# Kernel optimization log

Measured on AMD Instinct MI355X. Metric: run time of the kernel, lower is better.

Reference implementation:

```python
import jax, jax.numpy as jnp
import numpy as np
import math

B, T, M, C, H = 4, 1024, 256, 512, 8
HD = C // H
NEG = -1e30


def setup_inputs() -> dict:
    key = jax.random.key(0)
    ks = jax.random.split(key, 16)
    s = 1.0 / math.sqrt(C)
    inp = {
        'x': jax.random.normal(ks[0], (B, T, C), jnp.float32),
        'y': jax.random.normal(ks[1], (B, M, C), jnp.float32),
        'attn_x_mask': jnp.tril(jnp.ones((T, T), bool))[None, None],  # causal (1,1,T,T)
        'Wqkv_x': jax.random.normal(ks[2], (C, 3 * C), jnp.float32) * s,
        'bqkv_x': jnp.zeros((3 * C,), jnp.float32),
        'Wqkv_y': jax.random.normal(ks[3], (C, 3 * C), jnp.float32) * s,
        'bqkv_y': jnp.zeros((3 * C,), jnp.float32),
        'w4x': jax.random.normal(ks[4], (H, HD), jnp.float32) * math.sqrt(1.0 / C / 3),
        'w4y': jax.random.normal(ks[5], (H, HD), jnp.float32) * math.sqrt(1.0 / C / 3),
        'w4xy': jax.random.normal(ks[6], (H, HD), jnp.float32) * math.sqrt(1.0 / C / 3),
        'Wgs': jax.random.normal(ks[7], (C, C), jnp.float32) * s,
        'bgs': jnp.zeros((C,), jnp.float32),
        'Wgc': jax.random.normal(ks[8], (C, C), jnp.float32) * s,
        'bgc': jnp.zeros((C,), jnp.float32),
        'Wp': jax.random.normal(ks[9], (C, C), jnp.float32) * s,
        'bp': jnp.zeros((C,), jnp.float32),
    }
    return inp


def _heads(t):
    b, n, c = t.shape
    return t.reshape(b, n, H, HD).transpose(0, 2, 1, 3)  # (B,H,N,HD)


def reference(x, y, attn_x_mask, Wqkv_x, bqkv_x, Wqkv_y, bqkv_y,
              w4x, w4y, w4xy, Wgs, bgs, Wgc, bgc, Wp, bp):
    q_x, k_x, v_x = [_heads(t) for t in jnp.split(x @ Wqkv_x + bqkv_x, 3, axis=-1)]
    q_y, k_y, v_y = [_heads(t) for t in jnp.split(y @ Wqkv_y + bqkv_y, 3, axis=-1)]
    scale = 1.0 / math.sqrt(HD)

    # additive bias attention: catt1 (per query-x), catt2 (per key-y), catt3 (bilinear)
    catt1 = jnp.einsum('bhtd,hd->bht', q_x, w4x)[..., :, None]          # (B,H,T,1)
    catt2 = jnp.einsum('bhmd,hd->bhm', q_y, w4y)[:, :, None, :]          # (B,H,1,M)
    catt3 = jnp.einsum('bhtd,bhmd->bhtm', q_x * w4xy[None, :, None, :], k_y) * scale
    catt = catt1 + catt2 + catt3                                         # (B,H,T,M)

    catt_x2y = jax.nn.softmax(catt, axis=-1)
    catt_y2x = jax.nn.softmax(catt, axis=-2)

    cval_x2y = jnp.einsum('bhtm,bhmd->bhtd', catt_x2y, v_y)
    cval_x2y = cval_x2y.transpose(0, 2, 1, 3).reshape(B, T, C)

    # product-of-attentions: (T,M) @ (M,T) -> (T,T)
    chain = jnp.einsum('bhtm,bhsm->bhts', catt_x2y, catt_y2x) * (1.0 / math.sqrt(M))
    chain = jnp.where(attn_x_mask, chain, NEG)
    chain = jax.nn.softmax(chain, axis=-1)
    cval_y2x = jnp.einsum('bhts,bhsd->bhtd', chain, v_x)
    cval_y2x = cval_y2x.transpose(0, 2, 1, 3).reshape(B, T, C)

    cval = cval_x2y + cval_y2x + x

    # masked self-attention
    satt = jnp.einsum('bhtd,bhsd->bhts', q_x, k_x) * scale
    satt = jnp.where(attn_x_mask, satt, NEG)
    satt = jax.nn.softmax(satt, axis=-1)
    sval = jnp.einsum('bhts,bhsd->bhtd', satt, v_x).transpose(0, 2, 1, 3).reshape(B, T, C)

    sgate = jax.nn.sigmoid(sval @ Wgs + bgs)
    cgate = jax.nn.sigmoid(cval @ Wgc + bgc)
    out = (sgate * cval + cgate * sval) @ Wp + bp
    return out
```

## Files before the change

### kernel.cpp

```cpp
#include <hip/hip_runtime.h>
#include <hip/hip_bf16.h>

typedef __hip_bfloat16 bf16;
using f4 = __attribute__((ext_vector_type(4))) float;
using s8 = __attribute__((ext_vector_type(8))) short;
using s4 = __attribute__((ext_vector_type(4))) short;

__device__ __forceinline__ void storeOut(float* p, float v) { *p = v; }
__device__ __forceinline__ void storeOut(bf16* p, float v) { *p = __float2bfloat16(v); }
__device__ __forceinline__ short bfs(float x) { return __builtin_bit_cast(short, __float2bfloat16(x)); }

constexpr int B_ = 4, T_ = 1024, M_ = 256, C_ = 512, H_ = 8, HD_ = 64, C3_ = 1536;

#define MFMA16(a, b, c) __builtin_amdgcn_mfma_f32_16x16x32_bf16((a), (b), (c), 0, 0, 0)

__global__ __launch_bounds__(256) void prep_kernel(
    const float* __restrict__ Wqkv_x, const float* __restrict__ Wqkv_y,
    const float* __restrict__ Wgs, const float* __restrict__ Wgc, const float* __restrict__ Wp,
    const float* __restrict__ x, const float* __restrict__ y,
    bf16* __restrict__ WT_x, bf16* __restrict__ WT_y, bf16* __restrict__ WT_gs,
    bf16* __restrict__ WT_gc, bf16* __restrict__ WT_p,
    bf16* __restrict__ x_bf, bf16* __restrict__ y_bf)
{
    __shared__ float Ls[64][65];
    const int tid = threadIdx.x;
    const int bid = blockIdx.x;
    if (bid < 576) {
        const float* W; bf16* WT; int N, t;
        if (bid < 192)      { W = Wqkv_x; WT = WT_x;  N = C3_; t = bid; }
        else if (bid < 384) { W = Wqkv_y; WT = WT_y;  N = C3_; t = bid - 192; }
        else if (bid < 448) { W = Wgs;    WT = WT_gs; N = C_;  t = bid - 384; }
        else if (bid < 512) { W = Wgc;    WT = WT_gc; N = C_;  t = bid - 448; }
        else                { W = Wp;     WT = WT_p;  N = C_;  t = bid - 512; }
        const int K = C_;
        const int tw = N >> 6;
        const int n0 = (t % tw) * 64, k0 = (t / tw) * 64;
        for (int i = tid; i < 1024; i += 256) {
            int kr = i >> 4, ng = i & 15;
            float4 v = *(const float4*)&W[(size_t)(k0 + kr) * N + n0 + ng * 4];
            Ls[ng * 4 + 0][kr] = v.x; Ls[ng * 4 + 1][kr] = v.y;
            Ls[ng * 4 + 2][kr] = v.z; Ls[ng * 4 + 3][kr] = v.w;
        }
        __syncthreads();
        for (int i = tid; i < 512; i += 256) {
            int n = i >> 3, kg = i & 7;
            s8 r;
            #pragma unroll
            for (int j = 0; j < 8; ++j) r[j] = bfs(Ls[n][kg * 8 + j]);
            *(s8*)&WT[(size_t)(n0 + n) * K + k0 + kg * 8] = r;
        }
    } else if (bid < 1600) {
        int i = (bid - 576) * 2048 + tid * 8;
        s8 r;
        #pragma unroll
        for (int j = 0; j < 8; ++j) r[j] = bfs(x[i + j]);
        *(s8*)&x_bf[i] = r;
    } else {
        int i = (bid - 1600) * 2048 + tid * 8;
        s8 r;
        #pragma unroll
        for (int j = 0; j < 8; ++j) r[j] = bfs(y[i + j]);
        *(s8*)&y_bf[i] = r;
    }
}

__global__ __launch_bounds__(256) void qwcatt_kernel(
    const bf16* __restrict__ qkv_x, const bf16* __restrict__ qkv_y,
    const float* __restrict__ w4x, const float* __restrict__ w4y,
    const float* __restrict__ w4xy,
    float* __restrict__ catt1b, float* __restrict__ catt2b, bf16* __restrict__ qw)
{
    const int bid = blockIdx.x;
    const int tid = threadIdx.x;
    if (bid < 160) {
        int i = bid * 256 + tid;
        const bf16* row; const float* w; float* out; int oi;
        if (i < 32768) {
            int bh = i >> 10, t = i & 1023, b = bh >> 3, h = bh & 7;
            row = qkv_x + (size_t)(b * T_ + t) * C3_ + h * HD_;
            w = w4x + h * HD_; out = catt1b; oi = i;
        } else {
            int j = i - 32768;
            int bh = j >> 8, m = j & 255, b = bh >> 3, h = bh & 7;
            row = qkv_y + (size_t)(b * M_ + m) * C3_ + h * HD_;
            w = w4y + h * HD_; out = catt2b; oi = j;
        }
        float s = 0.f;
        #pragma unroll
        for (int d = 0; d < HD_; ++d) s = fmaf(__bfloat162float(row[d]), w[d], s);
        out[oi] = s;
    } else {
        int o = ((bid - 160) * 256 + tid) * 8;
        int row = o >> 9, c = o & 511;
        const bf16* src = qkv_x + (size_t)row * C3_ + c;
        s8 r;
        #pragma unroll
        for (int j = 0; j < 8; ++j) r[j] = bfs(__bfloat162float(src[j]) * w4xy[c + j]);
        *(s8*)&qw[o] = r;
    }
}

template <typename OT>
__global__ __launch_bounds__(256) void gemm_staged_kernel(
    const bf16* __restrict__ A, const bf16* __restrict__ WT, const float* __restrict__ bias,
    OT* __restrict__ Cmat, int N, int K)
{
    __shared__ short Asb[128][72];
    __shared__ short Bsb[64][72];
    const int tid = threadIdx.x;
    const int wave = tid >> 6, lane = tid & 63;
    const int quad = lane >> 4, l16 = lane & 15;
    const int n0 = blockIdx.y * 64, m0 = blockIdx.x * 128;
    f4 acc[2][4];
    #pragma unroll
    for (int mt = 0; mt < 2; ++mt)
        #pragma unroll
        for (int nt = 0; nt < 4; ++nt) acc[mt][nt] = (f4)0.f;

    for (int k0 = 0; k0 < K; k0 += 64) {
        #pragma unroll
        for (int tl = 0; tl < 4; ++tl) {
            int g = tid + tl * 256, row = g >> 3, grp = g & 7;
            *(s8*)&Asb[row][grp * 8] = *(const s8*)&A[(size_t)(m0 + row) * K + k0 + grp * 8];
        }
        #pragma unroll
        for (int tl = 0; tl < 2; ++tl) {
            int g = tid + tl * 256, n = g >> 3, grp = g & 7;
            *(s8*)&Bsb[n][grp * 8] = *(const s8*)&WT[(size_t)(n0 + n) * K + k0 + grp * 8];
        }
        __syncthreads();
        #pragma unroll
        for (int ks = 0; ks < 2; ++ks) {
            s8 a0 = *(const s8*)&Asb[wave * 32 + l16][ks * 32 + quad * 8];
            s8 a1 = *(const s8*)&Asb[wave * 32 + 16 + l16][ks * 32 + quad * 8];
            #pragma unroll
            for (int nt = 0; nt < 4; ++nt) {
                s8 bv = *(const s8*)&Bsb[nt * 16 + l16][ks * 32 + quad * 8];
                acc[0][nt] = MFMA16(a0, bv, acc[0][nt]);
                acc[1][nt] = MFMA16(a1, bv, acc[1][nt]);
            }
        }
        __syncthreads();
    }
    #pragma unroll
    for (int mt = 0; mt < 2; ++mt)
        #pragma unroll
        for (int nt = 0; nt < 4; ++nt) {
            int col = n0 + nt * 16 + l16;
            float bb = bias[col];
            #pragma unroll
            for (int reg = 0; reg < 4; ++reg) {
                int row = m0 + wave * 32 + mt * 16 + quad * 4 + reg;
                storeOut(&Cmat[(size_t)row * N + col], acc[mt][nt][reg] + bb);
            }
        }
}

__global__ __launch_bounds__(256) void catt3r_kernel(
    const bf16* __restrict__ qw, const bf16* __restrict__ qkv_y,
    const float* __restrict__ catt1, const float* __restrict__ catt2,
    bf16* __restrict__ x2y, float* __restrict__ rowsum_, float* __restrict__ psum)
{
    __shared__ float redc[4][256];
    const int tid = threadIdx.x;
    const int wave = tid >> 6, lane = tid & 63;
    const int quad = lane >> 4, l16 = lane & 15;
    const int bh = blockIdx.x, b = bh >> 3, h = bh & 7;
    const int t0 = blockIdx.y * 64;
    f4 sc[4][4];
    #pragma unroll
    for (int mt = 0; mt < 4; ++mt)
        #pragma unroll
        for (int nt = 0; nt < 4; ++nt) sc[mt][nt] = (f4)0.f;

    const bf16* ap = qw + (size_t)(b * T_ + t0 + wave * 16 + l16) * C_ + h * HD_ + quad * 8;
    s8 a0 = *(const s8*)ap;
    s8 a1 = *(const s8*)(ap + 32);
    const bf16* bp = qkv_y + (size_t)(b * M_ + l16) * C3_ + C_ + h * HD_ + quad * 8;
    #pragma unroll
    for (int mt = 0; mt < 4; ++mt)
        #pragma unroll
        for (int nt = 0; nt < 4; ++nt) {
            const bf16* bq = bp + (size_t)(mt * 64 + nt * 16) * C3_;
            sc[mt][nt] = MFMA16(a0, *(const s8*)bq, sc[mt][nt]);
            sc[mt][nt] = MFMA16(a1, *(const s8*)(bq + 32), sc[mt][nt]);
        }

    float c1[4];
    #pragma unroll
    for (int reg = 0; reg < 4; ++reg)
        c1[reg] = catt1[bh * T_ + t0 + wave * 16 + quad * 4 + reg];
    #pragma unroll
    for (int mt = 0; mt < 4; ++mt)
        #pragma unroll
        for (int nt = 0; nt < 4; ++nt) {
            float c2 = catt2[bh * M_ + mt * 64 + nt * 16 + l16];
            #pragma unroll
            for (int reg = 0; reg < 4; ++reg)
                sc[mt][nt][reg] = __expf(sc[mt][nt][reg] * 0.125f + c1[reg] + c2);
        }

    #pragma unroll
    for (int reg = 0; reg < 4; ++reg) {
        float rs = 0.f;
        #pragma unroll
        for (int mt = 0; mt < 4; ++mt)
            #pragma unroll
            for (int nt = 0; nt < 4; ++nt) rs += sc[mt][nt][reg];
        rs += __shfl_xor(rs, 1); rs += __shfl_xor(rs, 2);
        rs += __shfl_xor(rs, 4); rs += __shfl_xor(rs, 8);
        const int t = t0 + wave * 16 + quad * 4 + reg;
        if (l16 == 0) rowsum_[bh * T_ + t] = rs;
        const float ri = 1.f / rs;
        #pragma unroll
        for (int mt = 0; mt < 4; ++mt)
            #pragma unroll
            for (int nt = 0; nt < 4; ++nt)
                x2y[((size_t)bh * T_ + t) * M_ + mt * 64 + nt * 16 + l16] =
                    __float2bfloat16(sc[mt][nt][reg] * ri);
    }

    #pragma unroll
    for (int mt = 0; mt < 4; ++mt)
        #pragma unroll
        for (int nt = 0; nt < 4; ++nt) {
            float es = sc[mt][nt][0] + sc[mt][nt][1] + sc[mt][nt][2] + sc[mt][nt][3];
            es += __shfl_xor(es, 16);
            es += __shfl_xor(es, 32);
            if (quad == 0) redc[wave][mt * 64 + nt * 16 + l16] = es;
        }
    __syncthreads();
    psum[((size_t)bh * 16 + blockIdx.y) * M_ + tid] =
        redc[0][tid] + redc[1][tid] + redc[2][tid] + redc[3][tid];
}

__global__ __launch_bounds__(256) void colfin_vtrans_kernel(
    const float* __restrict__ psum, float* __restrict__ colinv,
    const bf16* __restrict__ qkv_x, const bf16* __restrict__ qkv_y,
    bf16* __restrict__ vTx, bf16* __restrict__ vTy)
{
    __shared__ short Ls[64][68];
    const int tid = threadIdx.x;
    int bid = blockIdx.x;
    if (bid < 32) {
        const int bh = bid, m = tid;
        float s = 0.f;
        #pragma unroll
        for (int ch = 0; ch < 16; ++ch) s += psum[(bh * 16 + ch) * M_ + m];
        colinv[bh * M_ + m] = 1.f / s;
        return;
    }
    bid -= 32;
    const bf16* qkv; bf16* vT; int Nrows, bh, t0;
    if (bid < 512) { qkv = qkv_x; vT = vTx; Nrows = T_; bh = bid >> 4; t0 = (bid & 15) * 64; }
    else { bid -= 512; qkv = qkv_y; vT = vTy; Nrows = M_; bh = bid >> 2; t0 = (bid & 3) * 64; }
    const int b = bh >> 3, h = bh & 7;
    for (int i = tid; i < 4096; i += 256) {
        int tl = i >> 6, d = i & 63;
        Ls[d][tl] = __builtin_bit_cast(short,
            qkv[(size_t)(b * Nrows + t0 + tl) * C3_ + 2 * C_ + h * HD_ + d]);
    }
    __syncthreads();
    for (int i = tid; i < 4096; i += 256) {
        int d = i >> 6, tl = i & 63;
        vT[((size_t)bh * 64 + d) * Nrows + t0 + tl] = __builtin_bit_cast(bf16, Ls[d][tl]);
    }
}

__global__ __launch_bounds__(256) void y2xw_kernel(
    const bf16* __restrict__ x2y, const float* __restrict__ rowsum_,
    const float* __restrict__ colinv, bf16* __restrict__ y2x)
{
    const int i = (blockIdx.x * 256 + threadIdx.x) * 8;
    const int row = i >> 8, m = i & 255, bh = row >> 10;
    const float rs = rowsum_[row];
    s8 v = *(const s8*)&x2y[i];
    const float4 c0 = *(const float4*)&colinv[bh * M_ + m];
    const float4 c4 = *(const float4*)&colinv[bh * M_ + m + 4];
    float ci[8] = {c0.x, c0.y, c0.z, c0.w, c4.x, c4.y, c4.z, c4.w};
    s8 r;
    #pragma unroll
    for (int j = 0; j < 8; ++j)
        r[j] = bfs(__bfloat162float(__builtin_bit_cast(bf16, v[j])) * rs * ci[j]);
    *(s8*)&y2x[i] = r;
}

__global__ __launch_bounds__(512) void flash8_kernel(
    const bf16* __restrict__ x2y, const bf16* __restrict__ y2x,
    const bf16* __restrict__ vTx, const bf16* __restrict__ vTy,
    const bf16* __restrict__ qkv_x, const float* __restrict__ x,
    bf16* __restrict__ cval_bf, bf16* __restrict__ sval_bf)
{
    __shared__ short Kc[64][264];
    __shared__ short Ksf[64][72];
    __shared__ short Vb[64][72];
    __shared__ short Ps[8][16][68];
    const int tid = threadIdx.x;
    const int wave = tid >> 6, lane = tid & 63;
    const int quad = lane >> 4, l16 = lane & 15;
    const int bh = blockIdx.x, b = bh >> 3, h = bh & 7;
    const int p = blockIdx.y;
    const int jt = (wave < 4) ? p : (15 - p);
    const int rb = jt * 64 + (wave & 3) * 16;
    const int nst = 16 - p;

    s8 qc[8], qs[2];
    {
        const bf16* qp = x2y + (size_t)(bh * T_ + rb + l16) * M_ + quad * 8;
        #pragma unroll
        for (int f = 0; f < 8; ++f) qc[f] = *(const s8*)(qp + f * 32);
        const bf16* qsp = qkv_x + (size_t)(b * T_ + rb + l16) * C3_ + h * HD_ + quad * 8;
        qs[0] = *(const s8*)qsp;
        qs[1] = *(const s8*)(qsp + 32);
    }

    f4 ocv[4];
    #pragma unroll
    for (int dt = 0; dt < 4; ++dt) ocv[dt] = (f4)0.f;
    {
        const bf16* vb = vTy + (size_t)(bh * 64 + l16) * M_ + quad * 8;
        #pragma unroll
        for (int f = 0; f < 8; ++f)
            #pragma unroll
            for (int dt = 0; dt < 4; ++dt) {
                s8 bv = *(const s8*)(vb + (size_t)dt * 16 * M_ + f * 32);
                ocv[dt] = MFMA16(qc[f], bv, ocv[dt]);
            }
    }

    f4 oc[4], os_[4];
    float lc[4] = {0.f, 0.f, 0.f, 0.f}, ls_[4] = {0.f, 0.f, 0.f, 0.f};
    #pragma unroll
    for (int dt = 0; dt < 4; ++dt) { oc[dt] = (f4)0.f; os_[dt] = (f4)0.f; }

    #pragma unroll
    for (int tl = 0; tl < 4; ++tl) {
        int g = tid + tl * 512, row = g >> 5, grp = g & 31;
        *(s8*)&Kc[row][grp * 8] = *(const s8*)&y2x[(size_t)(bh * T_ + row) * M_ + grp * 8];
    }
    {
        int row = tid >> 3, grp = tid & 7;
        *(s8*)&Ksf[row][grp * 8] =
            *(const s8*)&qkv_x[(size_t)(b * T_ + row) * C3_ + C_ + h * HD_ + grp * 8];
        *(s8*)&Vb[row][grp * 8] = *(const s8*)&vTx[(size_t)(bh * 64 + row) * T_ + grp * 8];
    }
    __syncthreads();

    for (int st = 0; st < nst; ++st) {
        const int s0 = st * 64;
        const bool pf = (st + 1) < nst;
        s8 kcp[4], ksp, vp;
        if (pf) {
            const int sn = s0 + 64;
            #pragma unroll
            for (int tl = 0; tl < 4; ++tl) {
                int g = tid + tl * 512, row = g >> 5, grp = g & 31;
                kcp[tl] = *(const s8*)&y2x[(size_t)(bh * T_ + sn + row) * M_ + grp * 8];
            }
            int row = tid >> 3, grp = tid & 7;
            ksp = *(const s8*)&qkv_x[(size_t)(b * T_ + sn + row) * C3_ + C_ + h * HD_ + grp * 8];
            vp = *(const s8*)&vTx[(size_t)(bh * 64 + row) * T_ + sn + grp * 8];
        }
        if (st <= jt) {
            f4 sc[4];
            #pragma unroll
            for (int nt = 0; nt < 4; ++nt) sc[nt] = (f4)0.f;
            #pragma unroll
            for (int f = 0; f < 8; ++f)
                #pragma unroll
                for (int nt = 0; nt < 4; ++nt) {
                    s8 bv = *(const s8*)&Kc[nt * 16 + l16][f * 32 + quad * 8];
                    sc[nt] = MFMA16(qc[f], bv, sc[nt]);
                }
            f4 ss[4];
            #pragma unroll
            for (int nt = 0; nt < 4; ++nt) ss[nt] = (f4)0.f;
            #pragma unroll
            for (int f = 0; f < 2; ++f)
                #pragma unroll
                for (int nt = 0; nt < 4; ++nt) {
                    s8 bv = *(const s8*)&Ksf[nt * 16 + l16][f * 32 + quad * 8];
                    ss[nt] = MFMA16(qs[f], bv, ss[nt]);
                }
            #pragma unroll
            for (int reg = 0; reg < 4; ++reg) {
                const int t_g = rb + quad * 4 + reg;
                #pragma unroll
                for (int nt = 0; nt < 4; ++nt) {
                    float pv = (s0 + nt * 16 + l16 <= t_g) ? __expf(sc[nt][reg] * (1.f / 16.f)) : 0.f;
                    lc[reg] += pv;
                    Ps[wave][quad * 4 + reg][nt * 16 + l16] = bfs(pv);
                }
            }
            #pragma unroll
            for (int ks = 0; ks < 2; ++ks) {
                const short* pp = &Ps[wave][l16][ks * 32 + quad * 8];
                s4 alo = *(const s4*)pp;
                s4 ahi = *(const s4*)(pp + 4);
                s8 a;
                a[0] = alo[0]; a[1] = alo[1]; a[2] = alo[2]; a[3] = alo[3];
                a[4] = ahi[0]; a[5] = ahi[1]; a[6] = ahi[2]; a[7] = ahi[3];
                #pragma unroll
                for (int dt = 0; dt < 4; ++dt) {
                    s8 bv = *(const s8*)&Vb[dt * 16 + l16][ks * 32 + quad * 8];
                    oc[dt] = MFMA16(a, bv, oc[dt]);
                }
            }
            #pragma unroll
            for (int reg = 0; reg < 4; ++reg) {
                const int t_g = rb + quad * 4 + reg;
                #pragma unroll
                for (int nt = 0; nt < 4; ++nt) {
                    float pv = (s0 + nt * 16 + l16 <= t_g) ? __expf(ss[nt][reg] * 0.125f) : 0.f;
                    ls_[reg] += pv;
                    Ps[wave][quad * 4 + reg][nt * 16 + l16] = bfs(pv);
                }
            }
            #pragma unroll
            for (int ks = 0; ks < 2; ++ks) {
                const short* pp = &Ps[wave][l16][ks * 32 + quad * 8];
                s4 alo = *(const s4*)pp;
                s4 ahi = *(const s4*)(pp + 4);
                s8 a;
                a[0] = alo[0]; a[1] = alo[1]; a[2] = alo[2]; a[3] = alo[3];
                a[4] = ahi[0]; a[5] = ahi[1]; a[6] = ahi[2]; a[7] = ahi[3];
                #pragma unroll
                for (int dt = 0; dt < 4; ++dt) {
                    s8 bv = *(const s8*)&Vb[dt * 16 + l16][ks * 32 + quad * 8];
                    os_[dt] = MFMA16(a, bv, os_[dt]);
                }
            }
        }
        __syncthreads();
        if (pf) {
            #pragma unroll
            for (int tl = 0; tl < 4; ++tl) {
                int g = tid + tl * 512, row = g >> 5, grp = g & 31;
                *(s8*)&Kc[row][grp * 8] = kcp[tl];
            }
            int row = tid >> 3, grp = tid & 7;
            *(s8*)&Ksf[row][grp * 8] = ksp;
            *(s8*)&Vb[row][grp * 8] = vp;
        }
        __syncthreads();
    }

    #pragma unroll
    for (int reg = 0; reg < 4; ++reg) {
        float l1 = lc[reg], l2 = ls_[reg];
        l1 += __shfl_xor(l1, 1); l1 += __shfl_xor(l1, 2);
        l1 += __shfl_xor(l1, 4); l1 += __shfl_xor(l1, 8);
        l2 += __shfl_xor(l2, 1); l2 += __shfl_xor(l2, 2);
        l2 += __shfl_xor(l2, 4); l2 += __shfl_xor(l2, 8);
        const float i1 = 1.f / l1, i2 = 1.f / l2;
        const int t = rb + quad * 4 + reg;
        #pragma unroll
        for (int dt = 0; dt < 4; ++dt) {
            size_t idx = (size_t)(b * T_ + t) * C_ + h * HD_ + dt * 16 + l16;
            float cv = ocv[dt][reg] + oc[dt][reg] * i1 + x[idx];
            cval_bf[idx] = __float2bfloat16(cv);
            float sv = os_[dt][reg] * i2;
            sval_bf[idx] = __float2bfloat16(sv);
        }
    }
}

__global__ __launch_bounds__(256) void gatefuse_kernel(
    const bf16* __restrict__ svalb, const bf16* __restrict__ cvalb,
    const bf16* __restrict__ WTgs, const bf16* __restrict__ WTgc,
    const float* __restrict__ bgs, const float* __restrict__ bgc,
    bf16* __restrict__ gated)
{
    __shared__ short Sb[128][72], Cb[128][72], W1b[64][72], W2b[64][72];
    const int tid = threadIdx.x;
    const int wave = tid >> 6, lane = tid & 63;
    const int quad = lane >> 4, l16 = lane & 15;
    const int n0 = blockIdx.y * 64, m0 = blockIdx.x * 128;
    f4 aS[2][4], aC[2][4];
    #pragma unroll
    for (int mt = 0; mt < 2; ++mt)
        #pragma unroll
        for (int nt = 0; nt < 4; ++nt) { aS[mt][nt] = (f4)0.f; aC[mt][nt] = (f4)0.f; }

    for (int k0 = 0; k0 < C_; k0 += 64) {
        #pragma unroll
        for (int tl = 0; tl < 4; ++tl) {
            int g = tid + tl * 256, row = g >> 3, grp = g & 7;
            *(s8*)&Sb[row][grp * 8] = *(const s8*)&svalb[(size_t)(m0 + row) * C_ + k0 + grp * 8];
            *(s8*)&Cb[row][grp * 8] = *(const s8*)&cvalb[(size_t)(m0 + row) * C_ + k0 + grp * 8];
        }
        #pragma unroll
        for (int tl = 0; tl < 2; ++tl) {
            int g = tid + tl * 256, n = g >> 3, grp = g & 7;
            *(s8*)&W1b[n][grp * 8] = *(const s8*)&WTgs[(size_t)(n0 + n) * C_ + k0 + grp * 8];
            *(s8*)&W2b[n][grp * 8] = *(const s8*)&WTgc[(size_t)(n0 + n) * C_ + k0 + grp * 8];
        }
        __syncthreads();
        #pragma unroll
        for (int ks = 0; ks < 2; ++ks) {
            s8 s0f = *(const s8*)&Sb[wave * 32 + l16][ks * 32 + quad * 8];
            s8 s1f = *(const s8*)&Sb[wave * 32 + 16 + l16][ks * 32 + quad * 8];
            s8 c0f = *(const s8*)&Cb[wave * 32 + l16][ks * 32 + quad * 8];
            s8 c1f = *(const s8*)&Cb[wave * 32 + 16 + l16][ks * 32 + quad * 8];
            #pragma unroll
            for (int nt = 0; nt < 4; ++nt) {
                s8 w1 = *(const s8*)&W1b[nt * 16 + l16][ks * 32 + quad * 8];
                s8 w2 = *(const s8*)&W2b[nt * 16 + l16][ks * 32 + quad * 8];
                aS[0][nt] = MFMA16(s0f, w1, aS[0][nt]);
                aS[1][nt] = MFMA16(s1f, w1, aS[1][nt]);
                aC[0][nt] = MFMA16(c0f, w2, aC[0][nt]);
                aC[1][nt] = MFMA16(c1f, w2, aC[1][nt]);
            }
        }
        __syncthreads();
    }
    #pragma unroll
    for (int mt = 0; mt < 2; ++mt)
        #pragma unroll
        for (int nt = 0; nt < 4; ++nt) {
            int col = n0 + nt * 16 + l16;
            float b1 = bgs[col], b2 = bgc[col];
            #pragma unroll
            for (int reg = 0; reg < 4; ++reg) {
                int row = m0 + wave * 32 + mt * 16 + quad * 4 + reg;
                size_t idx = (size_t)row * C_ + col;
                float gs = 1.f / (1.f + __expf(-(aS[mt][nt][reg] + b1)));
                float gc = 1.f / (1.f + __expf(-(aC[mt][nt][reg] + b2)));
                float cvv = __bfloat162float(cvalb[idx]);
                float svv = __bfloat162float(svalb[idx]);
                gated[idx] = __float2bfloat16(gs * cvv + gc * svv);
            }
        }
}

extern "C" void kernel_launch(void* const* d_in, const int* in_sizes, int n_in,
                              void* d_out, int out_size, void* d_ws, size_t ws_size,
                              hipStream_t stream)
{
    const float* x      = (const float*)d_in[0];
    const float* y      = (const float*)d_in[1];
    const float* Wqkv_x = (const float*)d_in[3];
    const float* bqkv_x = (const float*)d_in[4];
    const float* Wqkv_y = (const float*)d_in[5];
    const float* bqkv_y = (const float*)d_in[6];
    const float* w4x    = (const float*)d_in[7];
    const float* w4y    = (const float*)d_in[8];
    const float* w4xy   = (const float*)d_in[9];
    const float* Wgs    = (const float*)d_in[10];
    const float* bgs    = (const float*)d_in[11];
    const float* Wgc    = (const float*)d_in[12];
    const float* bgc    = (const float*)d_in[13];
    const float* Wp     = (const float*)d_in[14];
    const float* bp     = (const float*)d_in[15];

    float* ws = (float*)d_ws;
    bf16*  qkv_x_bf = (bf16*)(ws + 0);
    bf16*  qkv_y_bf = (bf16*)(ws + 3145728);
    bf16*  gated_bf = (bf16*)(ws + 3932160);
    bf16*  cval_bf  = (bf16*)(ws + 5242880);
    bf16*  x2y_bf   = (bf16*)(ws + 12320768);
    bf16*  x_bf     = x2y_bf;
    bf16*  y_bf     = (bf16*)(ws + 13369344);
    bf16*  y2x_bf   = (bf16*)(ws + 16515072);
    bf16*  vTx_bf   = (bf16*)(ws + 20709376);
    bf16*  vTy_bf   = (bf16*)(ws + 21757952);
    float* psum_    = ws + 22020096;
    bf16*  qw_bf    = (bf16*)(ws + 26214400);
    bf16*  sval_bf  = qw_bf;
    bf16*  WT_x     = (bf16*)(ws + 27262976);
    bf16*  WT_y     = (bf16*)(ws + 27656192);
    bf16*  WT_gs    = (bf16*)(ws + 28049408);
    bf16*  WT_gc    = (bf16*)(ws + 28180480);
    bf16*  WT_p     = (bf16*)(ws + 28311552);
    float* catt1b   = ws + 28442624;
    float* catt2b   = ws + 28475392;
    float* colinv   = ws + 28483584;
    float* rowsum_  = ws + 28491776;

    prep_kernel<<<1856, 256, 0, stream>>>(
        Wqkv_x, Wqkv_y, Wgs, Wgc, Wp, x, y,
        WT_x, WT_y, WT_gs, WT_gc, WT_p, x_bf, y_bf);

    gemm_staged_kernel<bf16><<<dim3(32, 24), 256, 0, stream>>>(x_bf, WT_x, bqkv_x, qkv_x_bf, C3_, C_);
    gemm_staged_kernel<bf16><<<dim3(8, 24), 256, 0, stream>>>(y_bf, WT_y, bqkv_y, qkv_y_bf, C3_, C_);

    qwcatt_kernel<<<1184, 256, 0, stream>>>(
        qkv_x_bf, qkv_y_bf, w4x, w4y, w4xy, catt1b, catt2b, qw_bf);

    catt3r_kernel<<<dim3(32, 16), 256, 0, stream>>>(
        qw_bf, qkv_y_bf, catt1b, catt2b, x2y_bf, rowsum_, psum_);

    colfin_vtrans_kernel<<<672, 256, 0, stream>>>(psum_, colinv, qkv_x_bf, qkv_y_bf, vTx_bf, vTy_bf);

    y2xw_kernel<<<4096, 256, 0, stream>>>(x2y_bf, rowsum_, colinv, y2x_bf);

    flash8_kernel<<<dim3(32, 8), 512, 0, stream>>>(
        x2y_bf, y2x_bf, vTx_bf, vTy_bf, qkv_x_bf, x, cval_bf, sval_bf);

    gatefuse_kernel<<<dim3(32, 8), 256, 0, stream>>>(
        sval_bf, cval_bf, WT_gs, WT_gc, bgs, bgc, gated_bf);

    gemm_staged_kernel<float><<<dim3(32, 8), 256, 0, stream>>>(
        gated_bf, WT_p, bp, (float*)d_out, C_, C_);
}
```

Baseline: 223.0 us.

## Rework flash attention kernel: register P transpose, per-block query tiles, wave priority

Replaces the 512-thread paired-tile flash kernel with a 256-thread kernel where each block owns one 64-row query tile, launched heaviest-first. The MFMA operands are swapped so the score tile comes out transposed, and P is converted to bf16 and rearranged in registers via ds_bpermute instead of a shared-memory round trip. Causal masking is applied only on the diagonal tile, and s_setprio is raised around MFMA bursts. This removes LDS traffic and the per-element mask work but doubles the block count, so K/V tiles are reloaded per block rather than shared across two query tiles.

Measured after the change: 231.8 us. 4.0% more time.

```diff
diff --git a/kernel.cpp b/kernel.cpp
--- a/kernel.cpp
+++ b/kernel.cpp
@@ -5,6 +5,7 @@
 using f4 = __attribute__((ext_vector_type(4))) float;
 using s8 = __attribute__((ext_vector_type(8))) short;
 using s4 = __attribute__((ext_vector_type(4))) short;
+using u4v = __attribute__((ext_vector_type(4))) unsigned;
 
 __device__ __forceinline__ void storeOut(float* p, float v) { *p = v; }
 __device__ __forceinline__ void storeOut(bf16* p, float v) { *p = __float2bfloat16(v); }
@@ -285,7 +286,41 @@
     *(s8*)&y2x[i] = r;
 }
 
-__global__ __launch_bounds__(512) void flash8_kernel(
+__device__ __forceinline__ unsigned cvtpk(float lo, float hi) {
+    unsigned d;
+    asm("v_cvt_pk_bf16_f32 %0, %1, %2" : "=v"(d) : "v"(lo), "v"(hi));
+    return d;
+}
+
+__device__ __forceinline__ void ptrans(const f4* sc, int idx0, int idx1, int gsel,
+                                       s8& aw0, s8& aw1)
+{
+    unsigned pk[4][2];
+    #pragma unroll
+    for (int nt = 0; nt < 4; ++nt) {
+        pk[nt][0] = cvtpk(sc[nt][0], sc[nt][1]);
+        pk[nt][1] = cvtpk(sc[nt][2], sc[nt][3]);
+    }
+    unsigned r[4][2][2];
+    #pragma unroll
+    for (int nt = 0; nt < 4; ++nt)
+        #pragma unroll
+        for (int par = 0; par < 2; ++par) {
+            r[nt][par][0] = (unsigned)__builtin_amdgcn_ds_bpermute(idx0, (int)pk[nt][par]);
+            r[nt][par][1] = (unsigned)__builtin_amdgcn_ds_bpermute(idx1, (int)pk[nt][par]);
+        }
+    u4v w0, w1;
+    #pragma unroll
+    for (int jp = 0; jp < 4; ++jp) {
+        const int par = jp & 1, hh = jp >> 1;
+        w0[jp] = gsel ? r[1][par][hh] : r[0][par][hh];
+        w1[jp] = gsel ? r[3][par][hh] : r[2][par][hh];
+    }
+    aw0 = __builtin_bit_cast(s8, w0);
+    aw1 = __builtin_bit_cast(s8, w1);
+}
+
+__global__ __launch_bounds__(256) void flash9_kernel(
     const bf16* __restrict__ x2y, const bf16* __restrict__ y2x,
     const bf16* __restrict__ vTx, const bf16* __restrict__ vTy,
     const bf16* __restrict__ qkv_x, const float* __restrict__ x,
@@ -294,15 +329,16 @@
     __shared__ short Kc[64][264];
     __shared__ short Ksf[64][72];
     __shared__ short Vb[64][72];
-    __shared__ short Ps[8][16][68];
     const int tid = threadIdx.x;
     const int wave = tid >> 6, lane = tid & 63;
     const int quad = lane >> 4, l16 = lane & 15;
     const int bh = blockIdx.x, b = bh >> 3, h = bh & 7;
-    const int p = blockIdx.y;
-    const int jt = (wave < 4) ? p : (15 - p);
-    const int rb = jt * 64 + (wave & 3) * 16;
-    const int nst = 16 - p;
+    const int jt = (blockIdx.y < 8) ? (15 - (int)blockIdx.y) : ((int)blockIdx.y - 8);
+    const int rb = jt * 64 + wave * 16;
+    const int nst = jt + 1;
+    const int gsel = quad >> 1;
+    const int idx0 = (((quad & 1) * 2) * 16 + l16) * 4;
+    const int idx1 = (((quad & 1) * 2 + 1) * 16 + l16) * 4;
 
     s8 qc[8], qs[2];
     {
@@ -329,17 +365,18 @@
     }
 
     f4 oc[4], os_[4];
-    float lc[4] = {0.f, 0.f, 0.f, 0.f}, ls_[4] = {0.f, 0.f, 0.f, 0.f};
+    float lc = 0.f, ls = 0.f;
     #pragma unroll
     for (int dt = 0; dt < 4; ++dt) { oc[dt] = (f4)0.f; os_[dt] = (f4)0.f; }
 
     #pragma unroll
-    for (int tl = 0; tl < 4; ++tl) {
-        int g = tid + tl * 512, row = g >> 5, grp = g & 31;
+    for (int tl = 0; tl < 8; ++tl) {
+        int g = tid + tl * 256, row = g >> 5, grp = g & 31;
         *(s8*)&Kc[row][grp * 8] = *(const s8*)&y2x[(size_t)(bh * T_ + row) * M_ + grp * 8];
     }
-    {
-        int row = tid >> 3, grp = tid & 7;
+    #pragma unroll
+    for (int tl = 0; tl < 2; ++tl) {
+        int g = tid + tl * 256, row = g >> 3, grp = g & 7;
         *(s8*)&Ksf[row][grp * 8] =
             *(const s8*)&qkv_x[(size_t)(b * T_ + row) * C3_ + C_ + h * HD_ + grp * 8];
         *(s8*)&Vb[row][grp * 8] = *(const s8*)&vTx[(size_t)(bh * 64 + row) * T_ + grp * 8];
@@ -349,110 +386,112 @@
     for (int st = 0; st < nst; ++st) {
         const int s0 = st * 64;
         const bool pf = (st + 1) < nst;
-        s8 kcp[4], ksp, vp;
+        s8 kcp[8], ksp[2], vp[2];
         if (pf) {
             const int sn = s0 + 64;
             #pragma unroll
-            for (int tl = 0; tl < 4; ++tl) {
-                int g = tid + tl * 512, row = g >> 5, grp = g & 31;
+            for (int tl = 0; tl < 8; ++tl) {
+                int g = tid + tl * 256, row = g >> 5, grp = g & 31;
                 kcp[tl] = *(const s8*)&y2x[(size_t)(bh * T_ + sn + row) * M_ + grp * 8];
             }
-            int row = tid >> 3, grp = tid & 7;
-            ksp = *(const s8*)&qkv_x[(size_t)(b * T_ + sn + row) * C3_ + C_ + h * HD_ + grp * 8];
-            vp = *(const s8*)&vTx[(size_t)(bh * 64 + row) * T_ + sn + grp * 8];
-        }
-        if (st <= jt) {
+            #pragma unroll
+            for (int tl = 0; tl < 2; ++tl) {
+                int g = tid + tl * 256, row = g >> 3, grp = g & 7;
+                ksp[tl] = *(const s8*)&qkv_x[(size_t)(b * T_ + sn + row) * C3_ + C_ + h * HD_ + grp * 8];
+                vp[tl] = *(const s8*)&vTx[(size_t)(bh * 64 + row) * T_ + sn + grp * 8];
+            }
+        }
+        {
+            const bool diag = (st == jt);
+            const int t_l = rb + l16;
             f4 sc[4];
             #pragma unroll
             for (int nt = 0; nt < 4; ++nt) sc[nt] = (f4)0.f;
+            __builtin_amdgcn_s_setprio(1);
             #pragma unroll
             for (int f = 0; f < 8; ++f)
                 #pragma unroll
                 for (int nt = 0; nt < 4; ++nt) {
                     s8 bv = *(const s8*)&Kc[nt * 16 + l16][f * 32 + quad * 8];
-                    sc[nt] = MFMA16(qc[f], bv, sc[nt]);
+                    sc[nt] = MFMA16(bv, qc[f], sc[nt]);
                 }
+            __builtin_amdgcn_s_setprio(0);
             f4 ss[4];
             #pragma unroll
             for (int nt = 0; nt < 4; ++nt) ss[nt] = (f4)0.f;
+            __builtin_amdgcn_s_setprio(1);
             #pragma unroll
             for (int f = 0; f < 2; ++f)
                 #pragma unroll
                 for (int nt = 0; nt < 4; ++nt) {
                     s8 bv = *(const s8*)&Ksf[nt * 16 + l16][f * 32 + quad * 8];
-                    ss[nt] = MFMA16(qs[f], bv, ss[nt]);
+                    ss[nt] = MFMA16(bv, qs[f], ss[nt]);
                 }
-            #pragma unroll
-            for (int reg = 0; reg < 4; ++reg) {
-                const int t_g = rb + quad * 4 + reg;
+            __builtin_amdgcn_s_setprio(0);
+            #pragma unroll
+            for (int nt = 0; nt < 4; ++nt)
                 #pragma unroll
-                for (int nt = 0; nt < 4; ++nt) {
-                    float pv = (s0 + nt * 16 + l16 <= t_g) ? __expf(sc[nt][reg] * (1.f / 16.f)) : 0.f;
-                    lc[reg] += pv;
-                    Ps[wave][quad * 4 + reg][nt * 16 + l16] = bfs(pv);
+                for (int reg = 0; reg < 4; ++reg) {
+                    float e = __expf(sc[nt][reg] * 0.0625f);
+                    if (diag) e = (s0 + nt * 16 + quad * 4 + reg <= t_l) ? e : 0.f;
+                    lc += e;
+                    sc[nt][reg] = e;
                 }
-            }
-            #pragma unroll
-            for (int ks = 0; ks < 2; ++ks) {
-                const short* pp = &Ps[wave][l16][ks * 32 + quad * 8];
-                s4 alo = *(const s4*)pp;
-                s4 ahi = *(const s4*)(pp + 4);
-                s8 a;
-                a[0] = alo[0]; a[1] = alo[1]; a[2] = alo[2]; a[3] = alo[3];
-                a[4] = ahi[0]; a[5] = ahi[1]; a[6] = ahi[2]; a[7] = ahi[3];
+            s8 ac0, ac1;
+            ptrans(sc, idx0, idx1, gsel, ac0, ac1);
+            __builtin_amdgcn_s_setprio(1);
+            #pragma unroll
+            for (int dt = 0; dt < 4; ++dt) {
+                s8 bv0 = *(const s8*)&Vb[dt * 16 + l16][quad * 8];
+                oc[dt] = MFMA16(ac0, bv0, oc[dt]);
+                s8 bv1 = *(const s8*)&Vb[dt * 16 + l16][32 + quad * 8];
+                oc[dt] = MFMA16(ac1, bv1, oc[dt]);
+            }
+            __builtin_amdgcn_s_setprio(0);
+            #pragma unroll
+            for (int nt = 0; nt < 4; ++nt)
                 #pragma unroll
-                for (int dt = 0; dt < 4; ++dt) {
-                    s8 bv = *(const s8*)&Vb[dt * 16 + l16][ks * 32 + quad * 8];
-                    oc[dt] = MFMA16(a, bv, oc[dt]);
+                for (int reg = 0; reg < 4; ++reg) {
+                    float e = __expf(ss[nt][reg] * 0.125f);
+                    if (diag) e = (s0 + nt * 16 + quad * 4 + reg <= t_l) ? e : 0.f;
+                    ls += e;
+                    ss[nt][reg] = e;
                 }
-            }
-            #pragma unroll
-            for (int reg = 0; reg < 4; ++reg) {
-                const int t_g = rb + quad * 4 + reg;
-                #pragma unroll
-                for (int nt = 0; nt < 4; ++nt) {
-                    float pv = (s0 + nt * 16 + l16 <= t_g) ? __expf(ss[nt][reg] * 0.125f) : 0.f;
-                    ls_[reg] += pv;
-                    Ps[wave][quad * 4 + reg][nt * 16 + l16] = bfs(pv);
-                }
-            }
-            #pragma unroll
-            for (int ks = 0; ks < 2; ++ks) {
-                const short* pp = &Ps[wave][l16][ks * 32 + quad * 8];
-                s4 alo = *(const s4*)pp;
-                s4 ahi = *(const s4*)(pp + 4);
-                s8 a;
-                a[0] = alo[0]; a[1] = alo[1]; a[2] = alo[2]; a[3] = alo[3];
-                a[4] = ahi[0]; a[5] = ahi[1]; a[6] = ahi[2]; a[7] = ahi[3];
-                #pragma unroll
-                for (int dt = 0; dt < 4; ++dt) {
-                    s8 bv = *(const s8*)&Vb[dt * 16 + l16][ks * 32 + quad * 8];
-                    os_[dt] = MFMA16(a, bv, os_[dt]);
-                }
-            }
+            s8 as0, as1;
+            ptrans(ss, idx0, idx1, gsel, as0, as1);
+            __builtin_amdgcn_s_setprio(1);
+            #pragma unroll
+            for (int dt = 0; dt < 4; ++dt) {
+                s8 bv0 = *(const s8*)&Vb[dt * 16 + l16][quad * 8];
+                os_[dt] = MFMA16(as0, bv0, os_[dt]);
+                s8 bv1 = *(const s8*)&Vb[dt * 16 + l16][32 + quad * 8];
+                os_[dt] = MFMA16(as1, bv1, os_[dt]);
+            }
+            __builtin_amdgcn_s_setprio(0);
         }
         __syncthreads();
         if (pf) {
             #pragma unroll
-            for (int tl = 0; tl < 4; ++tl) {
-                int g = tid + tl * 512, row = g >> 5, grp = g & 31;
+            for (int tl = 0; tl < 8; ++tl) {
+                int g = tid + tl * 256, row = g >> 5, grp = g & 31;
                 *(s8*)&Kc[row][grp * 8] = kcp[tl];
             }
-            int row = tid >> 3, grp = tid & 7;
-            *(s8*)&Ksf[row][grp * 8] = ksp;
-            *(s8*)&Vb[row][grp * 8] = vp;
+            #pragma unroll
+            for (int tl = 0; tl < 2; ++tl) {
+                int g = tid + tl * 256, row = g >> 3, grp = g & 7;
+                *(s8*)&Ksf[row][grp * 8] = ksp[tl];
+                *(s8*)&Vb[row][grp * 8] = vp[tl];
+            }
         }
         __syncthreads();
     }
 
+    lc += __shfl_xor(lc, 16); lc += __shfl_xor(lc, 32);
+    ls += __shfl_xor(ls, 16); ls += __shfl_xor(ls, 32);
     #pragma unroll
     for (int reg = 0; reg < 4; ++reg) {
-        float l1 = lc[reg], l2 = ls_[reg];
-        l1 += __shfl_xor(l1, 1); l1 += __shfl_xor(l1, 2);
-        l1 += __shfl_xor(l1, 4); l1 += __shfl_xor(l1, 8);
-        l2 += __shfl_xor(l2, 1); l2 += __shfl_xor(l2, 2);
-        l2 += __shfl_xor(l2, 4); l2 += __shfl_xor(l2, 8);
-        const float i1 = 1.f / l1, i2 = 1.f / l2;
+        const float i1 = 1.f / __shfl(lc, quad * 4 + reg);
+        const float i2 = 1.f / __shfl(ls, quad * 4 + reg);
         const int t = rb + quad * 4 + reg;
         #pragma unroll
         for (int dt = 0; dt < 4; ++dt) {
@@ -571,7 +610,7 @@
     bf16*  WT_y     = (bf16*)(ws + 27656192);
     bf16*  WT_gs    = (bf16*)(ws + 28049408);
     bf16*  WT_gc    = (bf16*)(ws + 28180480);
-    bf16*  WT_p     = (bf16*)(ws + 28311552);
+    bf16*  WT_p    = (bf16*)(ws + 28311552);
     float* catt1b   = ws + 28442624;
     float* catt2b   = ws + 28475392;
     float* colinv   = ws + 28483584;
@@ -594,7 +633,7 @@
 
     y2xw_kernel<<<4096, 256, 0, stream>>>(x2y_bf, rowsum_, colinv, y2x_bf);
 
-    flash8_kernel<<<dim3(32, 8), 512, 0, stream>>>(
+    flash9_kernel<<<dim3(32, 16), 256, 0, stream>>>(
         x2y_bf, y2x_bf, vTx_bf, vTy_bf, qkv_x_bf, x, cval_bf, sval_bf);
 
     gatefuse_kernel<<<dim3(32, 8), 256, 0, stream>>>(
```

## Split paired causal flash blocks into one 4-wave block per query tile

Applied to the files above, without the earlier changes.

The flash kernel used to pair two query tiles (p and 15-p) in one 512-thread block so every block did equal causal work. Now each 256-thread block handles a single 64-row query tile, launched in descending-work order, and loops only over the key tiles that tile needs. This removes the idle waves in paired blocks and the shared key staging between two tiles. In exchange it doubles the block count and the key/value loads into shared memory, and work per block becomes uneven.

New measurement: 240.6 us. 1.08x slower.

```diff
diff --git a/kernel.cpp b/kernel.cpp
--- a/kernel.cpp
+++ b/kernel.cpp
@@ -285,7 +285,7 @@
     *(s8*)&y2x[i] = r;
 }
 
-__global__ __launch_bounds__(512) void flash8_kernel(
+__global__ __launch_bounds__(256) void flash10_kernel(
     const bf16* __restrict__ x2y, const bf16* __restrict__ y2x,
     const bf16* __restrict__ vTx, const bf16* __restrict__ vTy,
     const bf16* __restrict__ qkv_x, const float* __restrict__ x,
@@ -294,15 +294,14 @@
     __shared__ short Kc[64][264];
     __shared__ short Ksf[64][72];
     __shared__ short Vb[64][72];
-    __shared__ short Ps[8][16][68];
+    __shared__ short Ps[4][16][68];
     const int tid = threadIdx.x;
     const int wave = tid >> 6, lane = tid & 63;
     const int quad = lane >> 4, l16 = lane & 15;
     const int bh = blockIdx.x, b = bh >> 3, h = bh & 7;
-    const int p = blockIdx.y;
-    const int jt = (wave < 4) ? p : (15 - p);
-    const int rb = jt * 64 + (wave & 3) * 16;
-    const int nst = 16 - p;
+    const int jt = (blockIdx.y < 8) ? (15 - (int)blockIdx.y) : ((int)blockIdx.y - 8);
+    const int rb = jt * 64 + wave * 16;
+    const int nst = jt + 1;
 
     s8 qc[8], qs[2];
     {
@@ -334,12 +333,13 @@
     for (int dt = 0; dt < 4; ++dt) { oc[dt] = (f4)0.f; os_[dt] = (f4)0.f; }
 
     #pragma unroll
-    for (int tl = 0; tl < 4; ++tl) {
-        int g = tid + tl * 512, row = g >> 5, grp = g & 31;
+    for (int tl = 0; tl < 8; ++tl) {
+        int g = tid + tl * 256, row = g >> 5, grp = g & 31;
         *(s8*)&Kc[row][grp * 8] = *(const s8*)&y2x[(size_t)(bh * T_ + row) * M_ + grp * 8];
     }
-    {
-        int row = tid >> 3, grp = tid & 7;
+    #pragma unroll
+    for (int tl = 0; tl < 2; ++tl) {
+        int g = tid + tl * 256, row = g >> 3, grp = g & 7;
         *(s8*)&Ksf[row][grp * 8] =
             *(const s8*)&qkv_x[(size_t)(b * T_ + row) * C3_ + C_ + h * HD_ + grp * 8];
         *(s8*)&Vb[row][grp * 8] = *(const s8*)&vTx[(size_t)(bh * 64 + row) * T_ + grp * 8];
@@ -349,19 +349,22 @@
     for (int st = 0; st < nst; ++st) {
         const int s0 = st * 64;
         const bool pf = (st + 1) < nst;
-        s8 kcp[4], ksp, vp;
+        s8 kcp[8], ksp[2], vp[2];
         if (pf) {
             const int sn = s0 + 64;
             #pragma unroll
-            for (int tl = 0; tl < 4; ++tl) {
-                int g = tid + tl * 512, row = g >> 5, grp = g & 31;
+            for (int tl = 0; tl < 8; ++tl) {
+                int g = tid + tl * 256, row = g >> 5, grp = g & 31;
                 kcp[tl] = *(const s8*)&y2x[(size_t)(bh * T_ + sn + row) * M_ + grp * 8];
             }
-            int row = tid >> 3, grp = tid & 7;
-            ksp = *(const s8*)&qkv_x[(size_t)(b * T_ + sn + row) * C3_ + C_ + h * HD_ + grp * 8];
-            vp = *(const s8*)&vTx[(size_t)(bh * 64 + row) * T_ + sn + grp * 8];
-        }
-        if (st <= jt) {
+            #pragma unroll
+            for (int tl = 0; tl < 2; ++tl) {
+                int g = tid + tl * 256, row = g >> 3, grp = g & 7;
+                ksp[tl] = *(const s8*)&qkv_x[(size_t)(b * T_ + sn + row) * C3_ + C_ + h * HD_ + grp * 8];
+                vp[tl] = *(const s8*)&vTx[(size_t)(bh * 64 + row) * T_ + sn + grp * 8];
+            }
+        }
+        {
             f4 sc[4];
             #pragma unroll
             for (int nt = 0; nt < 4; ++nt) sc[nt] = (f4)0.f;
@@ -434,13 +437,16 @@
         __syncthreads();
         if (pf) {
             #pragma unroll
-            for (int tl = 0; tl < 4; ++tl) {
-                int g = tid + tl * 512, row = g >> 5, grp = g & 31;
+            for (int tl = 0; tl < 8; ++tl) {
+                int g = tid + tl * 256, row = g >> 5, grp = g & 31;
                 *(s8*)&Kc[row][grp * 8] = kcp[tl];
             }
-            int row = tid >> 3, grp = tid & 7;
-            *(s8*)&Ksf[row][grp * 8] = ksp;
-            *(s8*)&Vb[row][grp * 8] = vp;
+            #pragma unroll
+            for (int tl = 0; tl < 2; ++tl) {
+                int g = tid + tl * 256, row = g >> 3, grp = g & 7;
+                *(s8*)&Ksf[row][grp * 8] = ksp[tl];
+                *(s8*)&Vb[row][grp * 8] = vp[tl];
+            }
         }
         __syncthreads();
     }
@@ -571,7 +577,7 @@
     bf16*  WT_y     = (bf16*)(ws + 27656192);
     bf16*  WT_gs    = (bf16*)(ws + 28049408);
     bf16*  WT_gc    = (bf16*)(ws + 28180480);
-    bf16*  WT_p     = (bf16*)(ws + 28311552);
+    bf16*  WT_p    = (bf16*)(ws + 28311552);
     float* catt1b   = ws + 28442624;
     float* catt2b   = ws + 28475392;
     float* colinv   = ws + 28483584;
@@ -594,7 +600,7 @@
 
     y2xw_kernel<<<4096, 256, 0, stream>>>(x2y_bf, rowsum_, colinv, y2x_bf);
 
-    flash8_kernel<<<dim3(32, 8), 512, 0, stream>>>(
+    flash10_kernel<<<dim3(32, 16), 256, 0, stream>>>(
         x2y_bf, y2x_bf, vTx_bf, vTy_bf, qkv_x_bf, x, cval_bf, sval_bf);
 
     gatefuse_kernel<<<dim3(32, 8), 256, 0, stream>>>(
```

## Fuse qw scaling into catt3r and y2x scaling into flash kernel loads

Applied to the files above, without the earlier changes.

Removes the separate qw buffer pass by applying the w4xy scaling to the q_x fragments inside catt3r. Also removes the y2xw kernel by rescaling x2y tiles with rowsum and colinv while they are loaded in the flash kernel, so y2x is never written or read back. This saves two launches and a full-size intermediate round trip through memory. In exchange the flash kernel does more ALU work, keeps more registers live for the colinv values, and may lose occupancy.

Measured after the change: 226.1 us. No clear change (+1.4%).

```diff
diff --git a/kernel.cpp b/kernel.cpp
--- a/kernel.cpp
+++ b/kernel.cpp
@@ -67,37 +67,24 @@
 __global__ __launch_bounds__(256) void qwcatt_kernel(
     const bf16* __restrict__ qkv_x, const bf16* __restrict__ qkv_y,
     const float* __restrict__ w4x, const float* __restrict__ w4y,
-    const float* __restrict__ w4xy,
-    float* __restrict__ catt1b, float* __restrict__ catt2b, bf16* __restrict__ qw)
-{
-    const int bid = blockIdx.x;
-    const int tid = threadIdx.x;
-    if (bid < 160) {
-        int i = bid * 256 + tid;
-        const bf16* row; const float* w; float* out; int oi;
-        if (i < 32768) {
-            int bh = i >> 10, t = i & 1023, b = bh >> 3, h = bh & 7;
-            row = qkv_x + (size_t)(b * T_ + t) * C3_ + h * HD_;
-            w = w4x + h * HD_; out = catt1b; oi = i;
-        } else {
-            int j = i - 32768;
-            int bh = j >> 8, m = j & 255, b = bh >> 3, h = bh & 7;
-            row = qkv_y + (size_t)(b * M_ + m) * C3_ + h * HD_;
-            w = w4y + h * HD_; out = catt2b; oi = j;
-        }
-        float s = 0.f;
-        #pragma unroll
-        for (int d = 0; d < HD_; ++d) s = fmaf(__bfloat162float(row[d]), w[d], s);
-        out[oi] = s;
+    float* __restrict__ catt1b, float* __restrict__ catt2b)
+{
+    int i = blockIdx.x * 256 + threadIdx.x;
+    const bf16* row; const float* w; float* out; int oi;
+    if (i < 32768) {
+        int bh = i >> 10, t = i & 1023, b = bh >> 3, h = bh & 7;
+        row = qkv_x + (size_t)(b * T_ + t) * C3_ + h * HD_;
+        w = w4x + h * HD_; out = catt1b; oi = i;
     } else {
-        int o = ((bid - 160) * 256 + tid) * 8;
-        int row = o >> 9, c = o & 511;
-        const bf16* src = qkv_x + (size_t)row * C3_ + c;
-        s8 r;
-        #pragma unroll
-        for (int j = 0; j < 8; ++j) r[j] = bfs(__bfloat162float(src[j]) * w4xy[c + j]);
-        *(s8*)&qw[o] = r;
-    }
+        int j = i - 32768;
+        int bh = j >> 8, m = j & 255, b = bh >> 3, h = bh & 7;
+        row = qkv_y + (size_t)(b * M_ + m) * C3_ + h * HD_;
+        w = w4y + h * HD_; out = catt2b; oi = j;
+    }
+    float s = 0.f;
+    #pragma unroll
+    for (int d = 0; d < HD_; ++d) s = fmaf(__bfloat162float(row[d]), w[d], s);
+    out[oi] = s;
 }
 
 template <typename OT>
@@ -157,8 +144,9 @@
 }
 
 __global__ __launch_bounds__(256) void catt3r_kernel(
-    const bf16* __restrict__ qw, const bf16* __restrict__ qkv_y,
+    const bf16* __restrict__ qkv_x, const bf16* __restrict__ qkv_y,
     const float* __restrict__ catt1, const float* __restrict__ catt2,
+    const float* __restrict__ w4xy,
     bf16* __restrict__ x2y, float* __restrict__ rowsum_, float* __restrict__ psum)
 {
     __shared__ float redc[4][256];
@@ -173,9 +161,16 @@
         #pragma unroll
         for (int nt = 0; nt < 4; ++nt) sc[mt][nt] = (f4)0.f;
 
-    const bf16* ap = qw + (size_t)(b * T_ + t0 + wave * 16 + l16) * C_ + h * HD_ + quad * 8;
-    s8 a0 = *(const s8*)ap;
-    s8 a1 = *(const s8*)(ap + 32);
+    const bf16* ap = qkv_x + (size_t)(b * T_ + t0 + wave * 16 + l16) * C3_ + h * HD_ + quad * 8;
+    s8 a0r = *(const s8*)ap;
+    s8 a1r = *(const s8*)(ap + 32);
+    const float* wx = w4xy + h * HD_ + quad * 8;
+    s8 a0, a1;
+    #pragma unroll
+    for (int j = 0; j < 8; ++j) {
+        a0[j] = bfs(__bfloat162float(__builtin_bit_cast(bf16, a0r[j])) * wx[j]);
+        a1[j] = bfs(__bfloat162float(__builtin_bit_cast(bf16, a1r[j])) * wx[j + 32]);
+    }
     const bf16* bp = qkv_y + (size_t)(b * M_ + l16) * C3_ + C_ + h * HD_ + quad * 8;
     #pragma unroll
     for (int mt = 0; mt < 4; ++mt)
@@ -267,26 +262,17 @@
     }
 }
 
-__global__ __launch_bounds__(256) void y2xw_kernel(
-    const bf16* __restrict__ x2y, const float* __restrict__ rowsum_,
-    const float* __restrict__ colinv, bf16* __restrict__ y2x)
-{
-    const int i = (blockIdx.x * 256 + threadIdx.x) * 8;
-    const int row = i >> 8, m = i & 255, bh = row >> 10;
-    const float rs = rowsum_[row];
-    s8 v = *(const s8*)&x2y[i];
-    const float4 c0 = *(const float4*)&colinv[bh * M_ + m];
-    const float4 c4 = *(const float4*)&colinv[bh * M_ + m + 4];
-    float ci[8] = {c0.x, c0.y, c0.z, c0.w, c4.x, c4.y, c4.z, c4.w};
+__device__ __forceinline__ s8 scale8(s8 v, float rs, const float* ci) {
     s8 r;
     #pragma unroll
     for (int j = 0; j < 8; ++j)
         r[j] = bfs(__bfloat162float(__builtin_bit_cast(bf16, v[j])) * rs * ci[j]);
-    *(s8*)&y2x[i] = r;
-}
-
-__global__ __launch_bounds__(512) void flash8_kernel(
-    const bf16* __restrict__ x2y, const bf16* __restrict__ y2x,
+    return r;
+}
+
+__global__ __launch_bounds__(512) void flash13_kernel(
+    const bf16* __restrict__ x2y, const float* __restrict__ rowsum_,
+    const float* __restrict__ colinv,
     const bf16* __restrict__ vTx, const bf16* __restrict__ vTy,
     const bf16* __restrict__ qkv_x, const float* __restrict__ x,
     bf16* __restrict__ cval_bf, bf16* __restrict__ sval_bf)
@@ -304,6 +290,16 @@
     const int rb = jt * 64 + (wave & 3) * 16;
     const int nst = 16 - p;
 
+    float ci8[4][8];
+    #pragma unroll
+    for (int tl = 0; tl < 4; ++tl) {
+        int grp = (tid + tl * 512) & 31;
+        float4 c0 = *(const float4*)&colinv[bh * M_ + grp * 8];
+        float4 c4 = *(const float4*)&colinv[bh * M_ + grp * 8 + 4];
+        ci8[tl][0] = c0.x; ci8[tl][1] = c0.y; ci8[tl][2] = c0.z; ci8[tl][3] = c0.w;
+        ci8[tl][4] = c4.x; ci8[tl][5] = c4.y; ci8[tl][6] = c4.z; ci8[tl][7] = c4.w;
+    }
+
     s8 qc[8], qs[2];
     {
         const bf16* qp = x2y + (size_t)(bh * T_ + rb + l16) * M_ + quad * 8;
@@ -336,7 +332,9 @@
     #pragma unroll
     for (int tl = 0; tl < 4; ++tl) {
         int g = tid + tl * 512, row = g >> 5, grp = g & 31;
-        *(s8*)&Kc[row][grp * 8] = *(const s8*)&y2x[(size_t)(bh * T_ + row) * M_ + grp * 8];
+        s8 v = *(const s8*)&x2y[(size_t)(bh * T_ + row) * M_ + grp * 8];
+        float rs = rowsum_[bh * T_ + row];
+        *(s8*)&Kc[row][grp * 8] = scale8(v, rs, ci8[tl]);
     }
     {
         int row = tid >> 3, grp = tid & 7;
@@ -355,7 +353,9 @@
             #pragma unroll
             for (int tl = 0; tl < 4; ++tl) {
                 int g = tid + tl * 512, row = g >> 5, grp = g & 31;
-                kcp[tl] = *(const s8*)&y2x[(size_t)(bh * T_ + sn + row) * M_ + grp * 8];
+                s8 v = *(const s8*)&x2y[(size_t)(bh * T_ + sn + row) * M_ + grp * 8];
+                float rs = rowsum_[bh * T_ + sn + row];
+                kcp[tl] = scale8(v, rs, ci8[tl]);
             }
             int row = tid >> 3, grp = tid & 7;
             ksp = *(const s8*)&qkv_x[(size_t)(b * T_ + sn + row) * C3_ + C_ + h * HD_ + grp * 8];
@@ -561,7 +561,6 @@
     bf16*  x2y_bf   = (bf16*)(ws + 12320768);
     bf16*  x_bf     = x2y_bf;
     bf16*  y_bf     = (bf16*)(ws + 13369344);
-    bf16*  y2x_bf   = (bf16*)(ws + 16515072);
     bf16*  vTx_bf   = (bf16*)(ws + 20709376);
     bf16*  vTy_bf   = (bf16*)(ws + 21757952);
     float* psum_    = ws + 22020096;
@@ -571,7 +570,7 @@
     bf16*  WT_y     = (bf16*)(ws + 27656192);
     bf16*  WT_gs    = (bf16*)(ws + 28049408);
     bf16*  WT_gc    = (bf16*)(ws + 28180480);
-    bf16*  WT_p     = (bf16*)(ws + 28311552);
+    bf16*  WT_p    = (bf16*)(ws + 28311552);
     float* catt1b   = ws + 28442624;
     float* catt2b   = ws + 28475392;
     float* colinv   = ws + 28483584;
@@ -584,18 +583,16 @@
     gemm_staged_kernel<bf16><<<dim3(32, 24), 256, 0, stream>>>(x_bf, WT_x, bqkv_x, qkv_x_bf, C3_, C_);
     gemm_staged_kernel<bf16><<<dim3(8, 24), 256, 0, stream>>>(y_bf, WT_y, bqkv_y, qkv_y_bf, C3_, C_);
 
-    qwcatt_kernel<<<1184, 256, 0, stream>>>(
-        qkv_x_bf, qkv_y_bf, w4x, w4y, w4xy, catt1b, catt2b, qw_bf);
+    qwcatt_kernel<<<160, 256, 0, stream>>>(
+        qkv_x_bf, qkv_y_bf, w4x, w4y, catt1b, catt2b);
 
     catt3r_kernel<<<dim3(32, 16), 256, 0, stream>>>(
-        qw_bf, qkv_y_bf, catt1b, catt2b, x2y_bf, rowsum_, psum_);
+        qkv_x_bf, qkv_y_bf, catt1b, catt2b, w4xy, x2y_bf, rowsum_, psum_);
 
     colfin_vtrans_kernel<<<672, 256, 0, stream>>>(psum_, colinv, qkv_x_bf, qkv_y_bf, vTx_bf, vTy_bf);
 
-    y2xw_kernel<<<4096, 256, 0, stream>>>(x2y_bf, rowsum_, colinv, y2x_bf);
-
-    flash8_kernel<<<dim3(32, 8), 512, 0, stream>>>(
-        x2y_bf, y2x_bf, vTx_bf, vTy_bf, qkv_x_bf, x, cval_bf, sval_bf);
+    flash13_kernel<<<dim3(32, 8), 512, 0, stream>>>(
+        x2y_bf, rowsum_, colinv, vTx_bf, vTy_bf, qkv_x_bf, x, cval_bf, sval_bf);
 
     gatefuse_kernel<<<dim3(32, 8), 256, 0, stream>>>(
         sval_bf, cval_bf, WT_gs, WT_gc, bgs, bgc, gated_bf);
```
